# Kernel tuning notes

Hardware: AMD Instinct MI355X
Metric: run time of the kernel (lower is better)

The kernel has to match this reference:

```python
import jax, jax.numpy as jnp
import numpy as np

N_QUBITS = 10
N_LAYERS = 2
BATCH = 4096


def _apply_1q(state, U, w):
    """Apply a single-qubit gate U ((2,2) or (batch,2,2)) on wire w.
    state: (batch, 2,2,...,2) with axis w+1 for wire w (wire 0 = leftmost)."""
    s = jnp.moveaxis(state, w + 1, -1)
    if U.ndim == 2:
        s = jnp.einsum('ij,...j->...i', U, s)
    else:  # per-sample gate (AngleEmbedding)
        s = jnp.einsum('bij,b...j->b...i', U, s)
    return jnp.moveaxis(s, -1, w + 1)


def _apply_cnot(state, c, t):
    ax_c, ax_t = c + 1, t + 1
    s0 = jnp.take(state, jnp.array([0]), axis=ax_c)
    s1 = jnp.take(state, jnp.array([1]), axis=ax_c)
    s1 = jnp.flip(s1, axis=ax_t)  # X on target where control == 1
    return jnp.concatenate([s0, s1], axis=ax_c)


def _ry(theta):
    """RY gate; theta scalar -> (2,2), theta (batch,) -> (batch,2,2)."""
    c, s = jnp.cos(theta / 2), jnp.sin(theta / 2)
    return jnp.stack([jnp.stack([c, -s], -1), jnp.stack([s, c], -1)], -2).astype(jnp.complex64)


def _rot(phi, theta, omega):
    """PennyLane Rot(phi, theta, omega) = RZ(omega) @ RY(theta) @ RZ(phi)."""
    c, s = jnp.cos(theta / 2), jnp.sin(theta / 2)
    ep = jnp.exp(-0.5j * (phi + omega))
    em = jnp.exp(0.5j * (phi - omega))
    return jnp.stack([
        jnp.stack([ep * c, -em * s], -1),
        jnp.stack([jnp.conj(em) * s, jnp.conj(ep) * c], -1),
    ], -2).astype(jnp.complex64)


def _qcircuit(x, weights):
    batch, n = x.shape
    L = weights.shape[0]
    state = jnp.zeros((batch,) + (2,) * n, dtype=jnp.complex64)
    state = state.at[(slice(None),) + (0,) * n].set(1.0)
    # AngleEmbedding, rotation='Y'
    for w in range(n):
        state = _apply_1q(state, _ry(x[:, w]), w)
    # StronglyEntanglingLayers: Rot on each wire, then CNOT ring with range r
    for l in range(L):
        for w in range(n):
            state = _apply_1q(state, _rot(weights[l, w, 0], weights[l, w, 1], weights[l, w, 2]), w)
        r = (l % (n - 1)) + 1
        for w in range(n):
            state = _apply_cnot(state, w, (w + r) % n)
    probs = state.real ** 2 + state.imag ** 2
    zs = []
    for w in range(n):
        axes = tuple(a for a in range(1, n + 1) if a != w + 1)
        m = probs.sum(axis=axes)  # (batch, 2)
        zs.append(m[:, 0] - m[:, 1])  # <Z_w>
    return jnp.stack(zs, axis=1).astype(jnp.float32)  # (batch, n)


def setup_inputs() -> dict:
    key = jax.random.key(0)
    ks = jax.random.split(key, 6)
    x = jax.random.uniform(ks[0], (BATCH, N_QUBITS), dtype=jnp.float32, maxval=2 * np.pi)
    weights = jax.random.uniform(ks[1], (N_LAYERS, N_QUBITS, 3), dtype=jnp.float32, maxval=2 * np.pi)
    w1 = jax.random.normal(ks[2], (8, N_QUBITS), dtype=jnp.float32) * 0.3
    b1 = jax.random.normal(ks[3], (8,), dtype=jnp.float32) * 0.1
    w2 = jax.random.normal(ks[4], (1, 8), dtype=jnp.float32) * 0.3
    b2 = jax.random.normal(ks[5], (1,), dtype=jnp.float32) * 0.1
    return {"x": x, "weights": weights, "w1": w1, "b1": b1, "w2": w2, "b2": b2}


def reference(x, weights, w1, b1, w2, b2):
    q = _qcircuit(x, weights)                 # (batch, n_qubits)
    h = jax.nn.relu(q @ w1.T + b1)            # (batch, 8)
    return jax.nn.sigmoid(h @ w2.T + b2)      # (batch, 1)
```

## Files before the change

kernel.cpp:

```cpp
#include <hip/hip_runtime.h>
#include <math.h>

#define NQ 10
#define BATCH 4096
#define REGS 16
#define T_OFF 128

struct cplx { float r, i; };
__device__ __forceinline__ cplx cmul(cplx a, cplx b) {
    return { fmaf(a.r, b.r, -(a.i * b.i)), fmaf(a.r, b.i, a.i * b.r) };
}
__device__ __forceinline__ cplx csel(bool hi, cplx b, cplx a) { return hi ? b : a; }
__device__ __forceinline__ float shfx(float v, int m) { return __shfl_xor(v, m, 64); }

__global__ void precompute(const float* __restrict__ weights, float* __restrict__ ws) {
    int j = blockIdx.x * blockDim.x + threadIdx.x;
    if (j < NQ) {
        float phi0 = weights[j * 3 + 0];
        float th0  = weights[j * 3 + 1];
        float om0  = weights[j * 3 + 2];
        float th1  = weights[(NQ + j) * 3 + 1];
        float c0, s0, cp, sp, co, so, c1, s1;
        sincosf(0.5f * th0,  &s0, &c0);
        sincosf(0.5f * phi0, &sp, &cp);
        sincosf(0.5f * om0,  &so, &co);
        sincosf(0.5f * th1,  &s1, &c1);
        float* p = ws + j * 8;
        p[0] = c0; p[1] = s0; p[2] = cp; p[3] = sp;
        p[4] = co; p[5] = so; p[6] = c1; p[7] = s1;
    }
    float phase = 0.f;
    #pragma unroll
    for (int w = 0; w < NQ; ++w) {
        float h = 0.5f * weights[(NQ + w) * 3 + 0];
        phase += ((j >> (9 - w)) & 1) ? h : -h;
    }
    float ti, tr;
    sincosf(phase, &ti, &tr);
    ws[T_OFF + 2 * j]     = tr;
    ws[T_OFF + 2 * j + 1] = ti;
}

__device__ __forceinline__ void apply_ry(float* ar, float* ai, int b,
                                         float c, float s, int lane) {
    if (b < 4) {
        int m = 1 << b;
        #pragma unroll
        for (int r = 0; r < REGS; ++r) {
            if (!(r & m)) {
                int r1 = r | m;
                float a0r = ar[r],  a0i = ai[r];
                float a1r = ar[r1], a1i = ai[r1];
                ar[r]  = c * a0r - s * a1r;  ai[r]  = c * a0i - s * a1i;
                ar[r1] = s * a0r + c * a1r;  ai[r1] = s * a0i + c * a1i;
            }
        }
    } else {
        int lm = 1 << (b - 4);
        float ss = ((lane >> (b - 4)) & 1) ? s : -s;
        #pragma unroll
        for (int r = 0; r < REGS; ++r) {
            float pr = shfx(ar[r], lm);
            float pi = shfx(ai[r], lm);
            ar[r] = fmaf(ss, pr, c * ar[r]);
            ai[r] = fmaf(ss, pi, c * ai[r]);
        }
    }
}

__global__ __launch_bounds__(256) void qnn_kernel(
    const float* __restrict__ x, const float* __restrict__ ws,
    const float* __restrict__ w1, const float* __restrict__ b1,
    const float* __restrict__ w2, const float* __restrict__ b2,
    float* __restrict__ out)
{
    int tid  = blockIdx.x * blockDim.x + threadIdx.x;
    int wave = tid >> 6;
    int lane = tid & 63;

    float Ar = 0.f, Ai = 0.f, Br = 0.f, Bi = 0.f;
    if (lane < NQ) {
        float xv = x[wave * NQ + lane];
        float sx, cx;
        sincosf(0.5f * xv, &sx, &cx);
        const float* p = ws + lane * 8;
        float c0 = p[0], s0 = p[1], cp = p[2], sp = p[3], co = p[4], so = p[5];
        float u0r = cp * cx, u0i = -sp * cx;
        float u1r = cp * sx, u1i =  sp * sx;
        float ar_ = c0 * u0r - s0 * u1r, ai_ = c0 * u0i - s0 * u1i;
        float br_ = s0 * u0r + c0 * u1r, bi_ = s0 * u0i + c0 * u1i;
        Ar = ar_ * co + ai_ * so;  Ai = ai_ * co - ar_ * so;
        Br = br_ * co - bi_ * so;  Bi = bi_ * co + br_ * so;
    }

    cplx a0w{__shfl(Ar,0,64),__shfl(Ai,0,64)}, b0w{__shfl(Br,0,64),__shfl(Bi,0,64)};
    cplx a1w{__shfl(Ar,1,64),__shfl(Ai,1,64)}, b1w{__shfl(Br,1,64),__shfl(Bi,1,64)};
    cplx a2w{__shfl(Ar,2,64),__shfl(Ai,2,64)}, b2w{__shfl(Br,2,64),__shfl(Bi,2,64)};
    cplx a3w{__shfl(Ar,3,64),__shfl(Ai,3,64)}, b3w{__shfl(Br,3,64),__shfl(Bi,3,64)};
    cplx a4w{__shfl(Ar,4,64),__shfl(Ai,4,64)}, b4w{__shfl(Br,4,64),__shfl(Bi,4,64)};
    cplx a5w{__shfl(Ar,5,64),__shfl(Ai,5,64)}, b5w{__shfl(Br,5,64),__shfl(Bi,5,64)};
    cplx a6w{__shfl(Ar,6,64),__shfl(Ai,6,64)}, b6w{__shfl(Br,6,64),__shfl(Bi,6,64)};
    cplx a7w{__shfl(Ar,7,64),__shfl(Ai,7,64)}, b7w{__shfl(Br,7,64),__shfl(Bi,7,64)};
    cplx a8w{__shfl(Ar,8,64),__shfl(Ai,8,64)}, b8w{__shfl(Br,8,64),__shfl(Bi,8,64)};
    cplx a9w{__shfl(Ar,9,64),__shfl(Ai,9,64)}, b9w{__shfl(Br,9,64),__shfl(Bi,9,64)};

    bool L2 = __popc(lane & 0x18) & 1;
    bool L3 = __popc(lane & 0x0C) & 1;
    bool L4 = __popc(lane & 0x06) & 1;
    bool L5 = __popc(lane & 0x03) & 1;
    cplx lp = csel(L2, b2w, a2w);
    lp = cmul(lp, csel(L3, b3w, a3w));
    lp = cmul(lp, csel(L4, b4w, a4w));
    lp = cmul(lp, csel(L5, b5w, a5w));

    bool Lb5 = (lane >> 5) & 1;
    bool L45 = __popc(lane & 0x30) & 1;
    cplx A0 = cmul(csel(Lb5, b0w, a0w), csel(L45, b1w, a1w));
    cplx A1 = cmul(csel(!Lb5, b0w, a0w), csel(!L45, b1w, a1w));

    bool Lb0 = lane & 1;
    cplx B0 = csel(Lb0, b6w, a6w);
    cplx B1 = csel(!Lb0, b6w, a6w);

    cplx g00 = cmul(a8w, a9w), g01 = cmul(a8w, b9w);
    cplx g10 = cmul(b8w, a9w), g11 = cmul(b8w, b9w);
    cplx C[2][2][2];
    C[0][0][0] = cmul(a7w, g00); C[0][0][1] = cmul(a7w, g01);
    C[0][1][0] = cmul(a7w, g10); C[0][1][1] = cmul(a7w, g11);
    C[1][0][0] = cmul(b7w, g00); C[1][0][1] = cmul(b7w, g01);
    C[1][1][0] = cmul(b7w, g10); C[1][1][1] = cmul(b7w, g11);

    cplx LA0 = cmul(lp, A0), LA1 = cmul(lp, A1);
    cplx LAB[2][2];
    LAB[0][0] = cmul(LA0, B0); LAB[0][1] = cmul(LA0, B1);
    LAB[1][0] = cmul(LA1, B0); LAB[1][1] = cmul(LA1, B1);

    float ar[REGS], ai[REGS];
    const float4* Tp = (const float4*)(ws + T_OFF + lane * 32);
    #pragma unroll
    for (int k = 0; k < 8; ++k) {
        float4 q = Tp[k];
        #pragma unroll
        for (int h = 0; h < 2; ++h) {
            int r = 2 * k + h;
            int p7 = ((r >> 2) ^ (r >> 3)) & 1;
            int p8 = ((r >> 1) ^ (r >> 2)) & 1;
            int p9 = (r ^ (r >> 1)) & 1;
            cplx v = cmul(LAB[r & 1][(r >> 3) & 1], C[p7][p8][p9]);
            cplx t = h ? cplx{q.z, q.w} : cplx{q.x, q.y};
            v = cmul(v, t);
            ar[r] = v.r; ai[r] = v.i;
        }
    }

    #pragma unroll
    for (int v = 0; v < NQ; ++v) {
        float c1 = ws[v * 8 + 6];
        float s1 = ws[v * 8 + 7];
        apply_ry(ar, ai, 9 - v, c1, s1, lane);
    }

    float S0 = 0.f, S4 = 0.f, S5 = 0.f, S8 = 0.f, SA = 0.f;
    #pragma unroll
    for (int r = 0; r < REGS; ++r) {
        float p = fmaf(ar[r], ar[r], ai[r] * ai[r]);
        S0 += p;
        S4 += (__popc(r & 0x4) & 1) ? -p : p;
        S5 += (__popc(r & 0x5) & 1) ? -p : p;
        S8 += (__popc(r & 0x8) & 1) ? -p : p;
        SA += (__popc(r & 0xA) & 1) ? -p : p;
    }
    float z[NQ];
    z[0] = (__popc(lane & 0x0A) & 1) ? -SA : SA;
    z[1] = (__popc(lane & 0x05) & 1) ? -S5 : S5;
    z[2] = (__popc(lane & 0x28) & 1) ? -S0 : S0;
    z[3] = (__popc(lane & 0x14) & 1) ? -S0 : S0;
    z[4] = (__popc(lane & 0x2A) & 1) ? -S0 : S0;
    z[5] = (__popc(lane & 0x15) & 1) ? -S0 : S0;
    z[6] = (__popc(lane & 0x2A) & 1) ? -S8 : S8;
    z[7] = (__popc(lane & 0x15) & 1) ? -S4 : S4;
    z[8] = (__popc(lane & 0x2A) & 1) ? -SA : SA;
    z[9] = (__popc(lane & 0x15) & 1) ? -S5 : S5;

    #pragma unroll
    for (int off = 32; off >= 1; off >>= 1) {
        #pragma unroll
        for (int w = 0; w < NQ; ++w)
            z[w] += shfx(z[w], off);
    }

    if (lane == 0) {
        float acc2 = b2[0];
        #pragma unroll
        for (int j = 0; j < 8; ++j) {
            float h = b1[j];
            #pragma unroll
            for (int w = 0; w < NQ; ++w)
                h = fmaf(z[w], w1[j * NQ + w], h);
            h = fmaxf(h, 0.0f);
            acc2 = fmaf(h, w2[j], acc2);
        }
        out[wave] = 1.0f / (1.0f + expf(-acc2));
    }
}

extern "C" void kernel_launch(void* const* d_in, const int* in_sizes, int n_in,
                              void* d_out, int out_size, void* d_ws, size_t ws_size,
                              hipStream_t stream) {
    const float* x       = (const float*)d_in[0];
    const float* weights = (const float*)d_in[1];
    const float* w1      = (const float*)d_in[2];
    const float* b1      = (const float*)d_in[3];
    const float* w2      = (const float*)d_in[4];
    const float* b2      = (const float*)d_in[5];
    float* out = (float*)d_out;
    float* ws  = (float*)d_ws;

    precompute<<<4, 256, 0, stream>>>(weights, ws);

    int threads = 256;
    int blocks  = (BATCH * 64) / threads;
    qnn_kernel<<<blocks, threads, 0, stream>>>(x, ws, w1, b1, w2, b2, out);
}
```

Before: 80.14 us.

## Replace statevector simulation with Heisenberg-picture Pauli propagation per sample

The 64-lane statevector simulation per sample is replaced by one thread per sample. Each thread evaluates every Z observable by propagating it backwards as Pauli strings through the CNOT ring (conjugation resolved at compile time through templates) and the final rotation layer, then contracting with Bloch vectors of the product state after embedding and the first rotation. This removes the many cross-lane shuffles and the 16-register state per lane, and the MLP now runs in every thread. The risks are a large amount of unrolled template code, which raises register pressure and code size, and only 64 blocks of 64 threads, which leaves much of the GPU idle.

```diff
diff --git a/kernel.cpp b/kernel.cpp
--- a/kernel.cpp
+++ b/kernel.cpp
@@ -3,205 +3,149 @@
 
 #define NQ 10
 #define BATCH 4096
-#define REGS 16
-#define T_OFF 128
 
-struct cplx { float r, i; };
-__device__ __forceinline__ cplx cmul(cplx a, cplx b) {
-    return { fmaf(a.r, b.r, -(a.i * b.i)), fmaf(a.r, b.i, a.i * b.r) };
-}
-__device__ __forceinline__ cplx csel(bool hi, cplx b, cplx a) { return hi ? b : a; }
-__device__ __forceinline__ float shfx(float v, int m) { return __shfl_xor(v, m, 64); }
 
-__global__ void precompute(const float* __restrict__ weights, float* __restrict__ ws) {
-    int j = blockIdx.x * blockDim.x + threadIdx.x;
-    if (j < NQ) {
-        float phi0 = weights[j * 3 + 0];
-        float th0  = weights[j * 3 + 1];
-        float om0  = weights[j * 3 + 2];
-        float th1  = weights[(NQ + j) * 3 + 1];
-        float c0, s0, cp, sp, co, so, c1, s1;
-        sincosf(0.5f * th0,  &s0, &c0);
-        sincosf(0.5f * phi0, &sp, &cp);
-        sincosf(0.5f * om0,  &so, &co);
-        sincosf(0.5f * th1,  &s1, &c1);
-        float* p = ws + j * 8;
-        p[0] = c0; p[1] = s0; p[2] = cp; p[3] = sp;
-        p[4] = co; p[5] = so; p[6] = c1; p[7] = s1;
-    }
-    float phase = 0.f;
-    #pragma unroll
-    for (int w = 0; w < NQ; ++w) {
-        float h = 0.5f * weights[(NQ + w) * 3 + 0];
-        phase += ((j >> (9 - w)) & 1) ? h : -h;
-    }
-    float ti, tr;
-    sincosf(phase, &ti, &tr);
-    ws[T_OFF + 2 * j]     = tr;
-    ws[T_OFF + 2 * j + 1] = ti;
+struct CR { int c, t, flip; };
+__host__ __device__ constexpr CR cnot_conj(int lc, int lt) {
+    const int xc = lc & 1, zc = (lc >> 1) & 1;
+    const int xt = lt & 1, zt = (lt >> 1) & 1;
+    const int flip = xc & zt & ((xt ^ zc) ^ 1);
+    const int nxt = xt ^ xc;
+    const int nzc = zc ^ zt;
+    return { (nzc << 1) | xc, (zt << 1) | nxt, flip };
 }
 
-__device__ __forceinline__ void apply_ry(float* ar, float* ai, int b,
-                                         float c, float s, int lane) {
-    if (b < 4) {
-        int m = 1 << b;
-        #pragma unroll
-        for (int r = 0; r < REGS; ++r) {
-            if (!(r & m)) {
-                int r1 = r | m;
-                float a0r = ar[r],  a0i = ai[r];
-                float a1r = ar[r1], a1i = ai[r1];
-                ar[r]  = c * a0r - s * a1r;  ai[r]  = c * a0i - s * a1i;
-                ar[r1] = s * a0r + c * a1r;  ai[r1] = s * a0i + c * a1i;
-            }
-        }
+template<int SM, int K, int L1, int L0, int F>
+__device__ __forceinline__ float chain(const float (&B)[NQ][4], const float (&C)[NQ][4], float p) {
+    if constexpr (K == 0) {
+        constexpr CR r = cnot_conj(L0, L1);
+        float v = p;
+        if constexpr (r.t != 0) v *= B[1][r.t];
+        if constexpr (r.c != 0) v *= B[0][r.c];
+        if constexpr (F ^ r.flip) return -v; else return v;
+    } else if constexpr ((SM >> K) & 1) {
+        float s = 0.f;
+        {   constexpr CR r = cnot_conj(1, L1);
+            float p2 = p * C[K][1];
+            if constexpr (r.t != 0) p2 *= B[K + 1][r.t];
+            s += chain<SM, K - 1, r.c, L0, F ^ r.flip>(B, C, p2); }
+        {   constexpr CR r = cnot_conj(2, L1);
+            float p2 = p * C[K][2];
+            if constexpr (r.t != 0) p2 *= B[K + 1][r.t];
+            s += chain<SM, K - 1, r.c, L0, F ^ r.flip>(B, C, p2); }
+        {   constexpr CR r = cnot_conj(3, L1);
+            float p2 = p * C[K][3];
+            if constexpr (r.t != 0) p2 *= B[K + 1][r.t];
+            s += chain<SM, K - 1, r.c, L0, F ^ r.flip>(B, C, p2); }
+        return s;
     } else {
-        int lm = 1 << (b - 4);
-        float ss = ((lane >> (b - 4)) & 1) ? s : -s;
-        #pragma unroll
-        for (int r = 0; r < REGS; ++r) {
-            float pr = shfx(ar[r], lm);
-            float pi = shfx(ai[r], lm);
-            ar[r] = fmaf(ss, pr, c * ar[r]);
-            ai[r] = fmaf(ss, pi, c * ai[r]);
-        }
+        constexpr CR r = cnot_conj(0, L1);
+        float p2 = p;
+        if constexpr (r.t != 0) p2 *= B[K + 1][r.t];
+        return chain<SM, K - 1, r.c, L0, F ^ r.flip>(B, C, p2);
     }
 }
 
-__global__ __launch_bounds__(256) void qnn_kernel(
+template<int SM, int S0, int S9>
+__device__ __forceinline__ float top2(const float (&B)[NQ][4], const float (&C)[NQ][4]) {
+    constexpr CR r = cnot_conj(S9, S0);
+    float p = 1.f;
+    if constexpr (S0 != 0) p *= C[0][S0];
+    if constexpr (S9 != 0) p *= C[9][S9];
+    return chain<SM, 8, r.c, r.t, r.flip>(B, C, p);
+}
+template<int SM, int S0>
+__device__ __forceinline__ float sum9(const float (&B)[NQ][4], const float (&C)[NQ][4]) {
+    if constexpr ((SM >> 9) & 1)
+        return top2<SM, S0, 1>(B, C) + top2<SM, S0, 2>(B, C) + top2<SM, S0, 3>(B, C);
+    else
+        return top2<SM, S0, 0>(B, C);
+}
+template<int SM>
+__device__ __forceinline__ float obs_eval(const float (&B)[NQ][4], const float (&C)[NQ][4]) {
+    if constexpr (SM & 1)
+        return sum9<SM, 1>(B, C) + sum9<SM, 2>(B, C) + sum9<SM, 3>(B, C);
+    else
+        return sum9<SM, 0>(B, C);
+}
+
+__global__ void precompute(const float* __restrict__ weights, float* __restrict__ ws) {
+    int w = threadIdx.x;
+    if (w >= NQ) return;
+    float phi0 = weights[w * 3 + 0], th0 = weights[w * 3 + 1], om0 = weights[w * 3 + 2];
+    float phi1 = weights[(NQ + w) * 3 + 0], th1 = weights[(NQ + w) * 3 + 1];
+    float cp, sp_, co, so, ct, st;
+    sincosf(phi0, &sp_, &cp);
+    sincosf(th0,  &st,  &ct);
+    sincosf(om0,  &so,  &co);
+    ws[w * 6 + 0] = co * ct * cp - so * sp_;
+    ws[w * 6 + 1] = so * ct * cp + co * sp_;
+    ws[w * 6 + 2] = -st * cp;
+    ws[w * 6 + 3] = co * st;
+    ws[w * 6 + 4] = so * st;
+    ws[w * 6 + 5] = ct;
+    float c1p, s1p, c1t, s1t;
+    sincosf(phi1, &s1p, &c1p);
+    sincosf(th1,  &s1t, &c1t);
+    ws[120 + w] = -s1t * c1p;
+    ws[130 + w] =  c1t;
+    ws[140 + w] =  s1t * s1p;
+}
+
+__global__ __launch_bounds__(64) void qnn_kernel(
     const float* __restrict__ x, const float* __restrict__ ws,
     const float* __restrict__ w1, const float* __restrict__ b1,
     const float* __restrict__ w2, const float* __restrict__ b2,
     float* __restrict__ out)
 {
-    int tid  = blockIdx.x * blockDim.x + threadIdx.x;
-    int wave = tid >> 6;
-    int lane = tid & 63;
+    const int s = blockIdx.x * 64 + threadIdx.x;
 
-    float Ar = 0.f, Ai = 0.f, Br = 0.f, Bi = 0.f;
-    if (lane < NQ) {
-        float xv = x[wave * NQ + lane];
-        float sx, cx;
-        sincosf(0.5f * xv, &sx, &cx);
-        const float* p = ws + lane * 8;
-        float c0 = p[0], s0 = p[1], cp = p[2], sp = p[3], co = p[4], so = p[5];
-        float u0r = cp * cx, u0i = -sp * cx;
-        float u1r = cp * sx, u1i =  sp * sx;
-        float ar_ = c0 * u0r - s0 * u1r, ai_ = c0 * u0i - s0 * u1i;
-        float br_ = s0 * u0r + c0 * u1r, bi_ = s0 * u0i + c0 * u1i;
-        Ar = ar_ * co + ai_ * so;  Ai = ai_ * co - ar_ * so;
-        Br = br_ * co - bi_ * so;  Bi = bi_ * co + br_ * so;
-    }
-
-    cplx a0w{__shfl(Ar,0,64),__shfl(Ai,0,64)}, b0w{__shfl(Br,0,64),__shfl(Bi,0,64)};
-    cplx a1w{__shfl(Ar,1,64),__shfl(Ai,1,64)}, b1w{__shfl(Br,1,64),__shfl(Bi,1,64)};
-    cplx a2w{__shfl(Ar,2,64),__shfl(Ai,2,64)}, b2w{__shfl(Br,2,64),__shfl(Bi,2,64)};
-    cplx a3w{__shfl(Ar,3,64),__shfl(Ai,3,64)}, b3w{__shfl(Br,3,64),__shfl(Bi,3,64)};
-    cplx a4w{__shfl(Ar,4,64),__shfl(Ai,4,64)}, b4w{__shfl(Br,4,64),__shfl(Bi,4,64)};
-    cplx a5w{__shfl(Ar,5,64),__shfl(Ai,5,64)}, b5w{__shfl(Br,5,64),__shfl(Bi,5,64)};
-    cplx a6w{__shfl(Ar,6,64),__shfl(Ai,6,64)}, b6w{__shfl(Br,6,64),__shfl(Bi,6,64)};
-    cplx a7w{__shfl(Ar,7,64),__shfl(Ai,7,64)}, b7w{__shfl(Br,7,64),__shfl(Bi,7,64)};
-    cplx a8w{__shfl(Ar,8,64),__shfl(Ai,8,64)}, b8w{__shfl(Br,8,64),__shfl(Bi,8,64)};
-    cplx a9w{__shfl(Ar,9,64),__shfl(Ai,9,64)}, b9w{__shfl(Br,9,64),__shfl(Bi,9,64)};
-
-    bool L2 = __popc(lane & 0x18) & 1;
-    bool L3 = __popc(lane & 0x0C) & 1;
-    bool L4 = __popc(lane & 0x06) & 1;
-    bool L5 = __popc(lane & 0x03) & 1;
-    cplx lp = csel(L2, b2w, a2w);
-    lp = cmul(lp, csel(L3, b3w, a3w));
-    lp = cmul(lp, csel(L4, b4w, a4w));
-    lp = cmul(lp, csel(L5, b5w, a5w));
-
-    bool Lb5 = (lane >> 5) & 1;
-    bool L45 = __popc(lane & 0x30) & 1;
-    cplx A0 = cmul(csel(Lb5, b0w, a0w), csel(L45, b1w, a1w));
-    cplx A1 = cmul(csel(!Lb5, b0w, a0w), csel(!L45, b1w, a1w));
-
-    bool Lb0 = lane & 1;
-    cplx B0 = csel(Lb0, b6w, a6w);
-    cplx B1 = csel(!Lb0, b6w, a6w);
-
-    cplx g00 = cmul(a8w, a9w), g01 = cmul(a8w, b9w);
-    cplx g10 = cmul(b8w, a9w), g11 = cmul(b8w, b9w);
-    cplx C[2][2][2];
-    C[0][0][0] = cmul(a7w, g00); C[0][0][1] = cmul(a7w, g01);
-    C[0][1][0] = cmul(a7w, g10); C[0][1][1] = cmul(a7w, g11);
-    C[1][0][0] = cmul(b7w, g00); C[1][0][1] = cmul(b7w, g01);
-    C[1][1][0] = cmul(b7w, g10); C[1][1][1] = cmul(b7w, g11);
-
-    cplx LA0 = cmul(lp, A0), LA1 = cmul(lp, A1);
-    cplx LAB[2][2];
-    LAB[0][0] = cmul(LA0, B0); LAB[0][1] = cmul(LA0, B1);
-    LAB[1][0] = cmul(LA1, B0); LAB[1][1] = cmul(LA1, B1);
-
-    float ar[REGS], ai[REGS];
-    const float4* Tp = (const float4*)(ws + T_OFF + lane * 32);
+    float B[NQ][4];
+    float C[NQ][4];
+    const float2* xp = (const float2*)(x + s * NQ);
     #pragma unroll
-    for (int k = 0; k < 8; ++k) {
-        float4 q = Tp[k];
+    for (int h = 0; h < 5; ++h) {
+        float2 xv = xp[h];
         #pragma unroll
-        for (int h = 0; h < 2; ++h) {
-            int r = 2 * k + h;
-            int p7 = ((r >> 2) ^ (r >> 3)) & 1;
-            int p8 = ((r >> 1) ^ (r >> 2)) & 1;
-            int p9 = (r ^ (r >> 1)) & 1;
-            cplx v = cmul(LAB[r & 1][(r >> 3) & 1], C[p7][p8][p9]);
-            cplx t = h ? cplx{q.z, q.w} : cplx{q.x, q.y};
-            v = cmul(v, t);
-            ar[r] = v.r; ai[r] = v.i;
+        for (int g = 0; g < 2; ++g) {
+            int w = 2 * h + g;
+            float sx, cx;
+            sincosf(g ? xv.y : xv.x, &sx, &cx);
+            const float* q = ws + w * 6;
+            B[w][0] = 1.f;
+            B[w][1] = fmaf(sx, q[0], cx * q[3]);
+            B[w][3] = fmaf(sx, q[1], cx * q[4]);
+            B[w][2] = fmaf(sx, q[2], cx * q[5]);
+            C[w][0] = 1.f;
+            C[w][1] = ws[120 + w];
+            C[w][2] = ws[130 + w];
+            C[w][3] = ws[140 + w];
         }
     }
 
+    float z[NQ];
+    z[0] = obs_eval<0x154>(B, C);
+    z[1] = obs_eval<0x2A8>(B, C);
+    z[2] = obs_eval<0x005>(B, C);
+    z[3] = obs_eval<0x00A>(B, C);
+    z[4] = obs_eval<0x015>(B, C);
+    z[5] = obs_eval<0x02A>(B, C);
+    z[6] = obs_eval<0x055>(B, C);
+    z[7] = obs_eval<0x0AA>(B, C);
+    z[8] = obs_eval<0x155>(B, C);
+    z[9] = obs_eval<0x2AA>(B, C);
+
+    float acc2 = b2[0];
     #pragma unroll
-    for (int v = 0; v < NQ; ++v) {
-        float c1 = ws[v * 8 + 6];
-        float s1 = ws[v * 8 + 7];
-        apply_ry(ar, ai, 9 - v, c1, s1, lane);
-    }
-
-    float S0 = 0.f, S4 = 0.f, S5 = 0.f, S8 = 0.f, SA = 0.f;
-    #pragma unroll
-    for (int r = 0; r < REGS; ++r) {
-        float p = fmaf(ar[r], ar[r], ai[r] * ai[r]);
-        S0 += p;
-        S4 += (__popc(r & 0x4) & 1) ? -p : p;
-        S5 += (__popc(r & 0x5) & 1) ? -p : p;
-        S8 += (__popc(r & 0x8) & 1) ? -p : p;
-        SA += (__popc(r & 0xA) & 1) ? -p : p;
-    }
-    float z[NQ];
-    z[0] = (__popc(lane & 0x0A) & 1) ? -SA : SA;
-    z[1] = (__popc(lane & 0x05) & 1) ? -S5 : S5;
-    z[2] = (__popc(lane & 0x28) & 1) ? -S0 : S0;
-    z[3] = (__popc(lane & 0x14) & 1) ? -S0 : S0;
-    z[4] = (__popc(lane & 0x2A) & 1) ? -S0 : S0;
-    z[5] = (__popc(lane & 0x15) & 1) ? -S0 : S0;
-    z[6] = (__popc(lane & 0x2A) & 1) ? -S8 : S8;
-    z[7] = (__popc(lane & 0x15) & 1) ? -S4 : S4;
-    z[8] = (__popc(lane & 0x2A) & 1) ? -SA : SA;
-    z[9] = (__popc(lane & 0x15) & 1) ? -S5 : S5;
-
-    #pragma unroll
-    for (int off = 32; off >= 1; off >>= 1) {
+    for (int j = 0; j < 8; ++j) {
+        float h = b1[j];
         #pragma unroll
         for (int w = 0; w < NQ; ++w)
-            z[w] += shfx(z[w], off);
+            h = fmaf(z[w], w1[j * NQ + w], h);
+        h = fmaxf(h, 0.f);
+        acc2 = fmaf(h, w2[j], acc2);
     }
-
-    if (lane == 0) {
-        float acc2 = b2[0];
-        #pragma unroll
-        for (int j = 0; j < 8; ++j) {
-            float h = b1[j];
-            #pragma unroll
-            for (int w = 0; w < NQ; ++w)
-                h = fmaf(z[w], w1[j * NQ + w], h);
-            h = fmaxf(h, 0.0f);
-            acc2 = fmaf(h, w2[j], acc2);
-        }
-        out[wave] = 1.0f / (1.0f + expf(-acc2));
-    }
+    out[s] = 1.f / (1.f + expf(-acc2));
 }
 
 extern "C" void kernel_launch(void* const* d_in, const int* in_sizes, int n_in,
@@ -216,9 +160,6 @@
     float* out = (float*)d_out;
     float* ws  = (float*)d_ws;
 
-    precompute<<<4, 256, 0, stream>>>(weights, ws);
-
-    int threads = 256;
-    int blocks  = (BATCH * 64) / threads;
-    qnn_kernel<<<blocks, threads, 0, stream>>>(x, ws, w1, b1, w2, b2, out);
+    precompute<<<1, 64, 0, stream>>>(weights, ws);
+    qnn_kernel<<<BATCH / 64, 64, 0, stream>>>(x, ws, w1, b1, w2, b2, out);
 }
```

New measurement: 74.35 us. 7.2% less time.
